# Kernel optimization log

Measured on AMD Instinct MI355X. Metric: run time of the kernel, lower is better.

The kernel has to match this reference:

```python
import jax, jax.numpy as jnp
import numpy as np

# static multi-scale feature pyramid (strides 8/16/32/64 of ~800px input)
SPATIAL = ((100, 100), (50, 50), (25, 25), (13, 13))
L = 4          # num_levels
NH = 8         # num_heads
NP = 4         # num_points
E = 256        # embed_dim
HD = E // NH   # head dim = 32
NLAYERS = 6
FFN_DIM = 1024
T = sum(h * w for h, w in SPATIAL)  # 13294 total tokens
B = 2


def _layer_norm(x, g, b, eps=1e-5):
    m = jnp.mean(x, -1, keepdims=True)
    v = jnp.mean((x - m) ** 2, -1, keepdims=True)
    return (x - m) * jax.lax.rsqrt(v + eps) * g + b


def _get_reference_points(valid_ratios):
    # valid_ratios: [B, L, 2] (wx, hy)
    refs = []
    for lvl, (H_, W_) in enumerate(SPATIAL):
        ry, rx = jnp.meshgrid(
            jnp.linspace(0.5, H_ - 0.5, H_, dtype=jnp.float32),
            jnp.linspace(0.5, W_ - 0.5, W_, dtype=jnp.float32),
            indexing='ij')
        ry = ry.reshape(-1)[None] / (valid_ratios[:, None, lvl, 1] * H_)
        rx = rx.reshape(-1)[None] / (valid_ratios[:, None, lvl, 0] * W_)
        refs.append(jnp.stack([rx, ry], -1))            # [B, H*W, 2]
    ref = jnp.concatenate(refs, 1)                       # [B, T, 2]
    return ref[:, :, None] * valid_ratios[:, None]       # [B, T, L, 2]


def _msda(value, loc, attn_w):
    # value: [B, T, NH, HD]; loc: [B, Q, NH, L, NP, 2] in [0,1]; attn_w: [B, Q, NH, L, NP]
    Bv, Tv, H, D = value.shape
    Q = loc.shape[1]
    out = jnp.zeros((Bv, Q, H, D), value.dtype)
    start = 0
    for lvl, (h, w) in enumerate(SPATIAL):
        v = value[:, start:start + h * w].transpose(0, 2, 1, 3)  # [B, NH, hw, D]
        start += h * w
        g = loc[:, :, :, lvl]                                    # [B, Q, NH, NP, 2]
        # grid_sample semantics, align_corners=False: pixel = g*size - 0.5
        x = g[..., 0] * w - 0.5
        y = g[..., 1] * h - 0.5
        x0 = jnp.floor(x).astype(jnp.int32)
        y0 = jnp.floor(y).astype(jnp.int32)
        wx = x - x0
        wy = y - y0

        def corner(ix, iy, cw):
            valid = (ix >= 0) & (ix < w) & (iy >= 0) & (iy < h)
            idx = jnp.clip(iy, 0, h - 1) * w + jnp.clip(ix, 0, w - 1)  # [B,Q,NH,NP]
            idx_t = idx.transpose(0, 2, 1, 3).reshape(Bv, H, Q * NP)
            gath = jnp.take_along_axis(v, idx_t[..., None], axis=2)    # [B,NH,QP,D]
            gath = gath.reshape(Bv, H, Q, NP, D)
            m = valid.transpose(0, 2, 1, 3)[..., None].astype(value.dtype)
            cw_t = cw.transpose(0, 2, 1, 3)[..., None]
            return gath * m * cw_t

        samp = (corner(x0, y0, (1 - wx) * (1 - wy))
                + corner(x0 + 1, y0, wx * (1 - wy))
                + corner(x0, y0 + 1, (1 - wx) * wy)
                + corner(x0 + 1, y0 + 1, wx * wy))  # [B,NH,Q,NP,D]
        out = out + jnp.einsum('bhqpd,bqhp->bqhd', samp, attn_w[:, :, :, lvl])
    return out.reshape(Bv, Q, H * D)


# offset normalizer (W, H) per level, as in Deformable-DETR
_OFF_NORM = jnp.array([[w, h] for (h, w) in SPATIAL], jnp.float32)  # [L, 2]


def _block(src, pos, ref, mask, p):
    (Wv, bv, Woff, boff, Wattn, battn, Wout, bout,
     n1g, n1b, n2g, n2b, W1, b1, W2, b2) = p
    x = _layer_norm(src, n1g, n1b)
    q = x + pos
    value = x @ Wv + bv
    value = jnp.where(mask[:, :, None], 0.0, value).reshape(B, T, NH, HD)
    off = (q @ Woff + boff).reshape(B, T, NH, L, NP, 2)
    attn = (q @ Wattn + battn).reshape(B, T, NH, L * NP)
    attn = jax.nn.softmax(attn, -1).reshape(B, T, NH, L, NP)
    loc = ref[:, :, None, :, None, :] + off / _OFF_NORM[None, None, None, :, None, :]
    attn_out = _msda(value, loc, attn) @ Wout + bout
    src = src + attn_out
    x = _layer_norm(src, n2g, n2b)
    ffn = jax.nn.relu(x @ W1 + b1) @ W2 + b2
    return src + ffn


def setup_inputs() -> dict:
    key = jax.random.key(0)
    ks = jax.random.split(key, 24)

    def rn(k, shape, scale=0.02):
        return jax.random.normal(k, shape, jnp.float32) * scale

    inp = {
        'src': jax.random.normal(ks[0], (B, T, E), jnp.float32),
        'pos': jax.random.normal(ks[1], (B, T, E), jnp.float32),
        'valid_ratios': jnp.ones((B, L, 2), jnp.float32),
        'spatial_shapes': jnp.array(SPATIAL, jnp.int32),
        'level_start_index': jnp.array(
            np.concatenate([[0], np.cumsum([h * w for h, w in SPATIAL])[:-1]]), jnp.int32),
        'mask': jnp.zeros((B, T), bool),
        # per-layer stacked parameters [NLAYERS, ...]
        'Wv': rn(ks[2], (NLAYERS, E, E)),
        'bv': jnp.zeros((NLAYERS, E), jnp.float32),
        'Woff': rn(ks[3], (NLAYERS, E, NH * L * NP * 2)),
        'boff': rn(ks[4], (NLAYERS, NH * L * NP * 2), 0.5),
        'Wattn': rn(ks[5], (NLAYERS, E, NH * L * NP)),
        'battn': jnp.zeros((NLAYERS, NH * L * NP), jnp.float32),
        'Wout': rn(ks[6], (NLAYERS, E, E)),
        'bout': jnp.zeros((NLAYERS, E), jnp.float32),
        'n1g': jnp.ones((NLAYERS, E), jnp.float32),
        'n1b': jnp.zeros((NLAYERS, E), jnp.float32),
        'n2g': jnp.ones((NLAYERS, E), jnp.float32),
        'n2b': jnp.zeros((NLAYERS, E), jnp.float32),
        'W1': rn(ks[7], (NLAYERS, E, FFN_DIM)),
        'b1': jnp.zeros((NLAYERS, FFN_DIM), jnp.float32),
        'W2': rn(ks[8], (NLAYERS, FFN_DIM, E)),
        'b2': jnp.zeros((NLAYERS, E), jnp.float32),
    }
    return inp


def reference(src, pos, valid_ratios, spatial_shapes, level_start_index, mask,
              Wv, bv, Woff, boff, Wattn, battn, Wout, bout,
              n1g, n1b, n2g, n2b, W1, b1, W2, b2):
    # spatial_shapes / level_start_index are encoded statically in SPATIAL (values match)
    ref = _get_reference_points(valid_ratios)  # [B, T, L, 2]
    x = src
    stacked = (Wv, bv, Woff, boff, Wattn, battn, Wout, bout,
               n1g, n1b, n2g, n2b, W1, b1, W2, b2)
    for i in range(NLAYERS):
        p = tuple(a[i] for a in stacked)
        x = _block(x, pos, ref, mask, p)
    return x
```

## Files before the change

### kernel.cpp

```cpp
#include <hip/hip_runtime.h>
#include <hip/hip_bf16.h>

#define NLAYERS 6
#define Bc 2
#define Tc 13294
#define Ec 256
#define NHc 8
#define FFNc 1024

#define EPI_BIAS 0
#define EPI_MASK 1
#define EPI_RES  2
#define EPI_RELU 3
#define EPI_VALOA 4

typedef __attribute__((ext_vector_type(8))) short bf16x8;
typedef __attribute__((ext_vector_type(4))) float f32x4;

typedef __attribute__((address_space(3))) unsigned int u32_lds;
typedef __attribute__((address_space(1))) unsigned int u32_glb;

__device__ __forceinline__ void gld16(const void* g, void* l) {
    __builtin_amdgcn_global_load_lds((const u32_glb*)g, (u32_lds*)l, 16, 0, 0);
}

__device__ __forceinline__ short f2bf(float f) {
    union { float f; unsigned u; } v; v.f = f;
    unsigned r = v.u + 0x7FFFu + ((v.u >> 16) & 1u);
    return (short)(r >> 16);
}
__device__ __forceinline__ float bf2f(short s) {
    union { unsigned u; float f; } v; v.u = ((unsigned)(unsigned short)s) << 16;
    return v.f;
}
__device__ __forceinline__ float bf_lo(unsigned u) {
    union { unsigned u; float f; } v; v.u = u << 16; return v.f;
}

__global__ __launch_bounds__(256) void f2bf_kernel(
    const float* __restrict__ in, short* __restrict__ out, int n4)
{
    int i = blockIdx.x * 256 + threadIdx.x;
    if (i >= n4) return;
    float4 v = *(const float4*)(in + (size_t)i * 4);
    short4 s; s.x = f2bf(v.x); s.y = f2bf(v.y); s.z = f2bf(v.z); s.w = f2bf(v.w);
    *(short4*)(out + (size_t)i * 4) = s;
}

__global__ __launch_bounds__(256) void ln_kernel(
    const float* __restrict__ src, const float* __restrict__ pos,
    const float* __restrict__ g, const float* __restrict__ b,
    short* __restrict__ x, short* __restrict__ q, int rows)
{
    int wave = threadIdx.x >> 6;
    int lane = threadIdx.x & 63;
    int row = blockIdx.x * 4 + wave;
    if (row >= rows) return;
    const float* p = src + (size_t)row * Ec;
    float4 v = *(const float4*)(p + lane * 4);
    float s  = v.x + v.y + v.z + v.w;
    float sq = v.x*v.x + v.y*v.y + v.z*v.z + v.w*v.w;
    #pragma unroll
    for (int o = 32; o; o >>= 1) { s += __shfl_xor(s, o); sq += __shfl_xor(sq, o); }
    float mean = s * (1.f / Ec);
    float var  = sq * (1.f / Ec) - mean * mean;
    float inv  = rsqrtf(var + 1e-5f);
    float4 gg = *(const float4*)(g + lane * 4);
    float4 bb = *(const float4*)(b + lane * 4);
    float xo0 = (v.x - mean) * inv * gg.x + bb.x;
    float xo1 = (v.y - mean) * inv * gg.y + bb.y;
    float xo2 = (v.z - mean) * inv * gg.z + bb.z;
    float xo3 = (v.w - mean) * inv * gg.w + bb.w;
    short4 xs; xs.x = f2bf(xo0); xs.y = f2bf(xo1); xs.z = f2bf(xo2); xs.w = f2bf(xo3);
    *(short4*)(x + (size_t)row * Ec + lane * 4) = xs;
    float4 pp = *(const float4*)(pos + (size_t)row * Ec + lane * 4);
    short4 qs;
    qs.x = f2bf(xo0 + pp.x); qs.y = f2bf(xo1 + pp.y);
    qs.z = f2bf(xo2 + pp.z); qs.w = f2bf(xo3 + pp.w);
    *(short4*)(q + (size_t)row * Ec + lane * 4) = qs;
}

__global__ __launch_bounds__(256) void ln_bf_kernel(
    const short* __restrict__ src, const short* __restrict__ pos,
    const float* __restrict__ g, const float* __restrict__ b,
    short* __restrict__ x, short* __restrict__ q, int rows)
{
    int wave = threadIdx.x >> 6;
    int lane = threadIdx.x & 63;
    int row = blockIdx.x * 4 + wave;
    if (row >= rows) return;
    short4 v4 = *(const short4*)(src + (size_t)row * Ec + lane * 4);
    float v0 = bf2f(v4.x), v1 = bf2f(v4.y), v2 = bf2f(v4.z), v3 = bf2f(v4.w);
    float s  = v0 + v1 + v2 + v3;
    float sq = v0*v0 + v1*v1 + v2*v2 + v3*v3;
    #pragma unroll
    for (int o = 32; o; o >>= 1) { s += __shfl_xor(s, o); sq += __shfl_xor(sq, o); }
    float mean = s * (1.f / Ec);
    float var  = sq * (1.f / Ec) - mean * mean;
    float inv  = rsqrtf(var + 1e-5f);
    float4 gg = *(const float4*)(g + lane * 4);
    float4 bb = *(const float4*)(b + lane * 4);
    float xo0 = (v0 - mean) * inv * gg.x + bb.x;
    float xo1 = (v1 - mean) * inv * gg.y + bb.y;
    float xo2 = (v2 - mean) * inv * gg.z + bb.z;
    float xo3 = (v3 - mean) * inv * gg.w + bb.w;
    short4 xs; xs.x = f2bf(xo0); xs.y = f2bf(xo1); xs.z = f2bf(xo2); xs.w = f2bf(xo3);
    *(short4*)(x + (size_t)row * Ec + lane * 4) = xs;
    if (q) {
        short4 pp = *(const short4*)(pos + (size_t)row * Ec + lane * 4);
        short4 qs;
        qs.x = f2bf(xo0 + bf2f(pp.x)); qs.y = f2bf(xo1 + bf2f(pp.y));
        qs.z = f2bf(xo2 + bf2f(pp.z)); qs.w = f2bf(xo3 + bf2f(pp.w));
        *(short4*)(q + (size_t)row * Ec + lane * 4) = qs;
    }
}

__global__ __launch_bounds__(256) void transpose_w(
    const float* __restrict__ W, short* __restrict__ Wt, int K, int N,
    int layerStride, int rowOff)
{
    __shared__ float tile[32][33];
    int l = blockIdx.z;
    const float* Wl = W + (size_t)l * K * N;
    short* Wtl = Wt + (size_t)l * layerStride;
    int n0 = blockIdx.x * 32, k0 = blockIdx.y * 32;
    int tx = threadIdx.x & 31, ty = threadIdx.x >> 5;
    #pragma unroll
    for (int i = 0; i < 32; i += 8)
        tile[ty + i][tx] = Wl[(size_t)(k0 + ty + i) * N + n0 + tx];
    __syncthreads();
    #pragma unroll
    for (int i = 0; i < 32; i += 8)
        Wtl[(size_t)(rowOff + n0 + ty + i) * K + k0 + tx] = f2bf(tile[tx][ty + i]);
}

template<int EPI, int OBF, int RESBF>
__global__ __launch_bounds__(256) void gemm_mfma(
    const short* __restrict__ A, const short* __restrict__ A2,
    const short* __restrict__ Bt,
    const float* __restrict__ bias, const float* __restrict__ bias2,
    const float* __restrict__ bias3,
    const float* __restrict__ resf, const short* __restrict__ resb,
    const unsigned char* __restrict__ mask,
    void* __restrict__ Cout, void* __restrict__ Cout2, int M, int N, int K)
{
    __shared__ short As[2][128 * 32];
    __shared__ short Bs[2][64 * 32];
    const int tid = threadIdx.x;
    const int lane = tid & 63;
    const int wv = tid >> 6;
    const int row0 = blockIdx.x * 128;
    const int col0 = blockIdx.y * 64;
    const int mbase = (wv >> 1) * 64;
    const int nbase = (wv & 1) * 32;
    const int lr = lane & 15;
    const int kg = lane >> 4;

    const short* Ause = (EPI == EPI_VALOA && blockIdx.y >= 4) ? A2 : A;

    f32x4 zf = {0.f, 0.f, 0.f, 0.f};
    f32x4 acc[4][2];
    #pragma unroll
    for (int i = 0; i < 4; ++i)
        #pragma unroll
        for (int j = 0; j < 2; ++j) acc[i][j] = zf;

    const int scol = (lane & 3) * 8;
    const int srowA = wv * 32 + (lane >> 2);
    const short* Ap = Ause + (size_t)(row0 + srowA) * K + scol;
    const int lA0 = srowA * 32 + scol;
    const int lA1 = lA0 + 16 * 32;
    const int srowB = wv * 16 + (lane >> 2);
    const short* Bp = Bt + (size_t)(col0 + srowB) * K + scol;
    const int lB = srowB * 32 + scol;

    #define STAGE(buf, k0) do { \
        gld16(Ap + (k0),                &As[buf][lA0]); \
        gld16(Ap + (size_t)16*K + (k0), &As[buf][lA1]); \
        gld16(Bp + (k0),                &Bs[buf][lB]); \
    } while (0)

    STAGE(0, 0);
    __syncthreads();
    int cur = 0;
    for (int k0 = 0; k0 < K; k0 += 32) {
        if (k0 + 32 < K) STAGE(cur ^ 1, k0 + 32);
        bf16x8 af[4], bfr[2];
        #pragma unroll
        for (int i = 0; i < 4; ++i)
            af[i]  = *(const bf16x8*)&As[cur][(mbase + i * 16 + lr) * 32 + kg * 8];
        #pragma unroll
        for (int j = 0; j < 2; ++j)
            bfr[j] = *(const bf16x8*)&Bs[cur][(nbase + j * 16 + lr) * 32 + kg * 8];
        #pragma unroll
        for (int mi = 0; mi < 4; ++mi)
            #pragma unroll
            for (int ni = 0; ni < 2; ++ni)
                acc[mi][ni] = __builtin_amdgcn_mfma_f32_16x16x32_bf16(
                    af[mi], bfr[ni], acc[mi][ni], 0, 0, 0);
        __syncthreads();
        cur ^= 1;
    }
    #undef STAGE

    float* Cf = (float*)Cout;
    short* Cb = (short*)Cout;
    short* Vb = (short*)Cout2;
    #pragma unroll
    for (int ni = 0; ni < 2; ++ni) {
        int col = col0 + nbase + ni * 16 + lr;
        float bz;
        if (EPI == EPI_VALOA)
            bz = (col < 256) ? bias[col] : ((col < 512) ? bias2[col - 256] : bias3[col - 512]);
        else
            bz = (bias2 && col >= 256) ? bias2[col - 256] : bias[col];
        #pragma unroll
        for (int mi = 0; mi < 4; ++mi) {
            int rb = row0 + mbase + mi * 16 + kg * 4;
            #pragma unroll
            for (int j = 0; j < 4; ++j) {
                int grow = rb + j;
                if (grow >= M) continue;
                float v = acc[mi][ni][j] + bz;
                if (EPI == EPI_VALOA) {
                    if (col < 256) {
                        if (mask[grow]) v = 0.f;
                        Vb[(size_t)grow * 256 + col] = f2bf(v);
                    } else {
                        Cb[(size_t)grow * 384 + (col - 256)] = f2bf(v);
                    }
                    continue;
                }
                if (EPI == EPI_MASK) { if (mask[grow]) v = 0.f; }
                if (EPI == EPI_RES) {
                    v += RESBF ? bf2f(resb[(size_t)grow * N + col])
                               : resf[(size_t)grow * N + col];
                }
                if (EPI == EPI_RELU) v = v > 0.f ? v : 0.f;
                if (OBF) Cb[(size_t)grow * N + col] = f2bf(v);
                else     Cf[(size_t)grow * N + col] = v;
            }
        }
    }
}

__global__ __launch_bounds__(256) void msda_kernel(
    const short* __restrict__ value, const short* __restrict__ oa,
    const float* __restrict__ vr, short* __restrict__ out)
{
    __shared__ int pts[8 * 136];
    const int t = threadIdx.x;
    const int bq = blockIdx.x;
    const int b = (bq >= Tc) ? 1 : 0;
    const int qq = bq - b * Tc;

    if (t < 128) {
        const int g = t >> 4;
        const int p = t & 15;
        const int lvl = p >> 2;
        const int Wl[4] = {100, 50, 25, 13};
        const int St[4] = {0, 10000, 12500, 13125};
        float base_x, base_y;
        if (qq < 10000) {
            int qi = qq;
            base_x = (0.5f + (float)(qi % 100)) / (vr[(b*4+0)*2+0] * 100.f);
            base_y = (0.5f + (float)(qi / 100)) / (vr[(b*4+0)*2+1] * 100.f);
        } else if (qq < 12500) {
            int qi = qq - 10000;
            base_x = (0.5f + (float)(qi % 50)) / (vr[(b*4+1)*2+0] * 50.f);
            base_y = (0.5f + (float)(qi / 50)) / (vr[(b*4+1)*2+1] * 50.f);
        } else if (qq < 13125) {
            int qi = qq - 12500;
            base_x = (0.5f + (float)(qi % 25)) / (vr[(b*4+2)*2+0] * 25.f);
            base_y = (0.5f + (float)(qi / 25)) / (vr[(b*4+2)*2+1] * 25.f);
        } else {
            int qi = qq - 13125;
            base_x = (0.5f + (float)(qi % 13)) / (vr[(b*4+3)*2+0] * 13.f);
            base_y = (0.5f + (float)(qi / 13)) / (vr[(b*4+3)*2+1] * 13.f);
        }
        float logit = bf2f(oa[(size_t)bq * 384 + 256 + g * 16 + p]);
        float mx = logit;
        #pragma unroll
        for (int o = 8; o; o >>= 1) mx = fmaxf(mx, __shfl_xor(mx, o));
        float e = expf(logit - mx);
        float sum = e;
        #pragma unroll
        for (int o = 8; o; o >>= 1) sum += __shfl_xor(sum, o);
        float aw = e / sum;

        const int w = Wl[lvl], hh = Wl[lvl];
        const float refx = base_x * vr[(b*4+lvl)*2+0];
        const float refy = base_y * vr[(b*4+lvl)*2+1];
        const float ox = bf2f(oa[(size_t)bq * 384 + g * 32 + p * 2 + 0]);
        const float oy = bf2f(oa[(size_t)bq * 384 + g * 32 + p * 2 + 1]);
        float locx = refx + ox / (float)w;
        float locy = refy + oy / (float)hh;
        float xf = locx * (float)w - 0.5f;
        float yf = locy * (float)hh - 0.5f;
        float x0f = floorf(xf), y0f = floorf(yf);
        int x0 = (int)x0f, y0 = (int)y0f;
        float wx = xf - x0f, wy = yf - y0f;
        float w00 = (1.f - wx) * (1.f - wy) * aw;
        float w10 = wx * (1.f - wy) * aw;
        float w01 = (1.f - wx) * wy * aw;
        float w11 = wx * wy * aw;
        bool vx0 = (x0 >= 0) && (x0 < w);
        bool vx1 = (x0 + 1 >= 0) && (x0 + 1 < w);
        bool vy0 = (y0 >= 0) && (y0 < hh);
        bool vy1 = (y0 + 1 >= 0) && (y0 + 1 < hh);
        if (!(vx0 && vy0)) w00 = 0.f;
        if (!(vx1 && vy0)) w10 = 0.f;
        if (!(vx0 && vy1)) w01 = 0.f;
        if (!(vx1 && vy1)) w11 = 0.f;
        int cx0 = min(max(x0, 0), w - 1), cx1 = min(max(x0 + 1, 0), w - 1);
        int cy0 = min(max(y0, 0), hh - 1), cy1 = min(max(y0 + 1, 0), hh - 1);
        int rowbase = b * Tc + St[lvl];
        int slot = g * 136 + p * 8 + ((p >> 3) & 1) * 4;
        int4 wq4; wq4.x = __float_as_int(w00); wq4.y = __float_as_int(w10);
        wq4.z = __float_as_int(w01); wq4.w = __float_as_int(w11);
        int4 aq4;
        aq4.x = (rowbase + cy0 * w + cx0) * 512 + g * 64;
        aq4.y = (rowbase + cy0 * w + cx1) * 512 + g * 64;
        aq4.z = (rowbase + cy1 * w + cx0) * 512 + g * 64;
        aq4.w = (rowbase + cy1 * w + cx1) * 512 + g * 64;
        *(int4*)&pts[slot] = wq4;
        *(int4*)&pts[slot + 4] = aq4;
    }
    __syncthreads();

    const int group = t >> 5;
    const int l32 = t & 31;
    const int d4 = (l32 & 15) * 4;
    const int ph = (l32 >> 4) * 8;
    const int xw = (l32 >> 4) * 4;
    const char* vbase = (const char*)value;
    float accL = 0.f, accH = 0.f;
    #pragma unroll
    for (int j = 0; j < 8; ++j) {
        int p = ph + j;
        int slot = group * 136 + p * 8 + xw;
        int4 wq = *(const int4*)&pts[slot];
        int4 aq = *(const int4*)&pts[slot + 4];
        unsigned u0 = *(const unsigned*)(vbase + (unsigned)(aq.x + d4));
        unsigned u1 = *(const unsigned*)(vbase + (unsigned)(aq.y + d4));
        unsigned u2 = *(const unsigned*)(vbase + (unsigned)(aq.z + d4));
        unsigned u3 = *(const unsigned*)(vbase + (unsigned)(aq.w + d4));
        float w00 = __int_as_float(wq.x), w10 = __int_as_float(wq.y);
        float w01 = __int_as_float(wq.z), w11 = __int_as_float(wq.w);
        accL = fmaf(w00, bf_lo(u0), accL); accH = fmaf(w00, __int_as_float((int)u0), accH);
        accL = fmaf(w10, bf_lo(u1), accL); accH = fmaf(w10, __int_as_float((int)u1), accH);
        accL = fmaf(w01, bf_lo(u2), accL); accH = fmaf(w01, __int_as_float((int)u2), accH);
        accL = fmaf(w11, bf_lo(u3), accL); accH = fmaf(w11, __int_as_float((int)u3), accH);
    }
    accL += __shfl_xor(accL, 16);
    accH += __shfl_xor(accH, 16);
    if (l32 < 16) {
        unsigned pk = ((unsigned)(unsigned short)f2bf(accL)) |
                      (((unsigned)(unsigned short)f2bf(accH)) << 16);
        *(unsigned*)((char*)out + (size_t)bq * 512 + group * 64 + d4) = pk;
    }
}

extern "C" void kernel_launch(void* const* d_in, const int* in_sizes, int n_in,
                              void* d_out, int out_size, void* d_ws, size_t ws_size,
                              hipStream_t stream) {
    const float* src  = (const float*)d_in[0];
    const float* pos  = (const float*)d_in[1];
    const float* vr   = (const float*)d_in[2];
    const unsigned char* mask = (const unsigned char*)d_in[5];
    const float* Wv    = (const float*)d_in[6];
    const float* bv    = (const float*)d_in[7];
    const float* Woff  = (const float*)d_in[8];
    const float* boff  = (const float*)d_in[9];
    const float* Wattn = (const float*)d_in[10];
    const float* battn = (const float*)d_in[11];
    const float* Wout  = (const float*)d_in[12];
    const float* bout  = (const float*)d_in[13];
    const float* n1g   = (const float*)d_in[14];
    const float* n1b   = (const float*)d_in[15];
    const float* n2g   = (const float*)d_in[16];
    const float* n2b   = (const float*)d_in[17];
    const float* W1    = (const float*)d_in[18];
    const float* b1    = (const float*)d_in[19];
    const float* W2    = (const float*)d_in[20];
    const float* b2    = (const float*)d_in[21];
    float* out = (float*)d_out;

    const size_t R = (size_t)Bc * Tc;

    short* xb    = (short*)d_ws;
    short* qb    = xb + R * 256;
    short* valb  = qb + R * 256;
    short* msdab = valb + R * 256;
    short* oab   = msdab + R * 256;
    short* srcb  = oab + R * 384;
    short* posb  = srcb + R * 256;
    short* ln2b  = xb;
    short* hb    = qb;
    short* wcT   = posb + R * 256;
    short* woutT = wcT + 6 * 163840;
    short* w1T   = woutT + 6 * 65536;
    short* w2T   = w1T + 6 * 262144;

    transpose_w<<<dim3(8, 8, 6),  256, 0, stream>>>(Wv,    wcT,   256, 256,  163840, 0);
    transpose_w<<<dim3(8, 8, 6),  256, 0, stream>>>(Woff,  wcT,   256, 256,  163840, 256);
    transpose_w<<<dim3(4, 8, 6),  256, 0, stream>>>(Wattn, wcT,   256, 128,  163840, 512);
    transpose_w<<<dim3(8, 8, 6),  256, 0, stream>>>(Wout,  woutT, 256, 256,  65536, 0);
    transpose_w<<<dim3(32, 8, 6), 256, 0, stream>>>(W1,    w1T,   256, 1024, 262144, 0);
    transpose_w<<<dim3(8, 32, 6), 256, 0, stream>>>(W2,    w2T,   1024, 256, 262144, 0);
    f2bf_kernel<<<(int)((R * 64 + 255) / 256), 256, 0, stream>>>(pos, posb, (int)(R * 64));

    const int M = (int)R;
    const int lnBlocks = (int)((R + 3) / 4);
    const int MT = (int)((R + 127) / 128);

    ln_kernel<<<lnBlocks, 256, 0, stream>>>(src, pos, n1g, n1b, xb, qb, M);

    for (int l = 0; l < NLAYERS; ++l) {
        gemm_mfma<EPI_VALOA, 1, 0><<<dim3(MT, 10), 256, 0, stream>>>(
            xb, qb, wcT + (size_t)l * 163840, bv + l * Ec, boff + l * 256, battn + l * 128,
            nullptr, nullptr, mask, oab, valb, M, 640, 256);
        msda_kernel<<<(int)R, 256, 0, stream>>>(valb, oab, vr, msdab);
        if (l == 0)
            gemm_mfma<EPI_RES, 1, 0><<<dim3(MT, 4), 256, 0, stream>>>(
                msdab, nullptr, woutT + (size_t)l * 65536, bout + l * Ec, nullptr, nullptr,
                src, nullptr, nullptr, srcb, nullptr, M, 256, 256);
        else
            gemm_mfma<EPI_RES, 1, 1><<<dim3(MT, 4), 256, 0, stream>>>(
                msdab, nullptr, woutT + (size_t)l * 65536, bout + l * Ec, nullptr, nullptr,
                nullptr, srcb, nullptr, srcb, nullptr, M, 256, 256);
        ln_bf_kernel<<<lnBlocks, 256, 0, stream>>>(srcb, nullptr, n2g + l * Ec, n2b + l * Ec,
                                                   ln2b, nullptr, M);
        gemm_mfma<EPI_RELU, 1, 0><<<dim3(MT, 16), 256, 0, stream>>>(
            ln2b, nullptr, w1T + (size_t)l * 262144, b1 + l * FFNc, nullptr, nullptr,
            nullptr, nullptr, nullptr, hb, nullptr, M, 1024, 256);
        if (l < NLAYERS - 1) {
            gemm_mfma<EPI_RES, 1, 1><<<dim3(MT, 4), 256, 0, stream>>>(
                hb, nullptr, w2T + (size_t)l * 262144, b2 + l * Ec, nullptr, nullptr,
                nullptr, srcb, nullptr, srcb, nullptr, M, 256, 1024);
            ln_bf_kernel<<<lnBlocks, 256, 0, stream>>>(srcb, posb, n1g + (l + 1) * Ec,
                                                       n1b + (l + 1) * Ec, xb, qb, M);
        } else {
            gemm_mfma<EPI_RES, 0, 1><<<dim3(MT, 4), 256, 0, stream>>>(
                hb, nullptr, w2T + (size_t)l * 262144, b2 + l * Ec, nullptr, nullptr,
                nullptr, srcb, nullptr, out, nullptr, M, 256, 1024);
        }
    }
}
```

Baseline: 1.151 ms.

## Add 128x128-tile GEMM for wide projections and widen MSDA value loads

Adds a gemm128 kernel with 128x128 output tiles (4x4 MFMA fragments per wave), used for the fused value/offset/attention projection and the FFN up-projection. The larger tiles give more reuse per staged A/B tile and halve the grid's column blocks. The MSDA sampling loop now loads 8 bytes per corner per lane instead of 4 and covers each head with 8 lanes, adding an extra shuffle-reduction step. The narrow-N GEMMs keep the slimmer 128x64 kernel. The cost is more accumulator registers, which may reduce occupancy.

```diff
diff --git a/kernel.cpp b/kernel.cpp
--- a/kernel.cpp
+++ b/kernel.cpp
@@ -136,13 +136,10 @@
 
 template<int EPI, int OBF, int RESBF>
 __global__ __launch_bounds__(256) void gemm_mfma(
-    const short* __restrict__ A, const short* __restrict__ A2,
-    const short* __restrict__ Bt,
-    const float* __restrict__ bias, const float* __restrict__ bias2,
-    const float* __restrict__ bias3,
+    const short* __restrict__ A, const short* __restrict__ Bt,
+    const float* __restrict__ bias,
     const float* __restrict__ resf, const short* __restrict__ resb,
-    const unsigned char* __restrict__ mask,
-    void* __restrict__ Cout, void* __restrict__ Cout2, int M, int N, int K)
+    void* __restrict__ Cout, int M, int N, int K)
 {
     __shared__ short As[2][128 * 32];
     __shared__ short Bs[2][64 * 32];
@@ -156,8 +153,6 @@
     const int lr = lane & 15;
     const int kg = lane >> 4;
 
-    const short* Ause = (EPI == EPI_VALOA && blockIdx.y >= 4) ? A2 : A;
-
     f32x4 zf = {0.f, 0.f, 0.f, 0.f};
     f32x4 acc[4][2];
     #pragma unroll
@@ -167,7 +162,7 @@
 
     const int scol = (lane & 3) * 8;
     const int srowA = wv * 32 + (lane >> 2);
-    const short* Ap = Ause + (size_t)(row0 + srowA) * K + scol;
+    const short* Ap = A + (size_t)(row0 + srowA) * K + scol;
     const int lA0 = srowA * 32 + scol;
     const int lA1 = lA0 + 16 * 32;
     const int srowB = wv * 16 + (lane >> 2);
@@ -205,15 +200,102 @@
 
     float* Cf = (float*)Cout;
     short* Cb = (short*)Cout;
-    short* Vb = (short*)Cout2;
     #pragma unroll
     for (int ni = 0; ni < 2; ++ni) {
+        int col = col0 + nbase + ni * 16 + lr;
+        float bz = bias[col];
+        #pragma unroll
+        for (int mi = 0; mi < 4; ++mi) {
+            int rb = row0 + mbase + mi * 16 + kg * 4;
+            #pragma unroll
+            for (int j = 0; j < 4; ++j) {
+                int grow = rb + j;
+                if (grow >= M) continue;
+                float v = acc[mi][ni][j] + bz;
+                if (EPI == EPI_RES) {
+                    v += RESBF ? bf2f(resb[(size_t)grow * N + col])
+                               : resf[(size_t)grow * N + col];
+                }
+                if (OBF) Cb[(size_t)grow * N + col] = f2bf(v);
+                else     Cf[(size_t)grow * N + col] = v;
+            }
+        }
+    }
+}
+
+template<int EPI>
+__global__ __launch_bounds__(256) void gemm128(
+    const short* __restrict__ A, const short* __restrict__ A2,
+    const short* __restrict__ Bt,
+    const float* __restrict__ bias, const float* __restrict__ bias2,
+    const float* __restrict__ bias3, const unsigned char* __restrict__ mask,
+    short* __restrict__ Cout, short* __restrict__ Vout, int M, int N, int K)
+{
+    __shared__ short As[2][128 * 32];
+    __shared__ short Bs[2][128 * 32];
+    const int tid = threadIdx.x;
+    const int lane = tid & 63;
+    const int wv = tid >> 6;
+    const int row0 = blockIdx.x * 128;
+    const int col0 = blockIdx.y * 128;
+    const int mbase = (wv >> 1) * 64;
+    const int nbase = (wv & 1) * 64;
+    const int lr = lane & 15;
+    const int kg = lane >> 4;
+
+    const short* Ause = (EPI == EPI_VALOA && blockIdx.y >= 2) ? A2 : A;
+
+    f32x4 zf = {0.f, 0.f, 0.f, 0.f};
+    f32x4 acc[4][4];
+    #pragma unroll
+    for (int i = 0; i < 4; ++i)
+        #pragma unroll
+        for (int j = 0; j < 4; ++j) acc[i][j] = zf;
+
+    const int scol = (lane & 3) * 8;
+    const int sr = wv * 32 + (lane >> 2);
+    const short* Ap = Ause + (size_t)(row0 + sr) * K + scol;
+    const short* Bp = Bt + (size_t)(col0 + sr) * K + scol;
+    const int l0 = sr * 32 + scol;
+    const int l1 = l0 + 16 * 32;
+
+    #define STAGE(buf, k0) do { \
+        gld16(Ap + (k0),                &As[buf][l0]); \
+        gld16(Ap + (size_t)16*K + (k0), &As[buf][l1]); \
+        gld16(Bp + (k0),                &Bs[buf][l0]); \
+        gld16(Bp + (size_t)16*K + (k0), &Bs[buf][l1]); \
+    } while (0)
+
+    STAGE(0, 0);
+    __syncthreads();
+    int cur = 0;
+    for (int k0 = 0; k0 < K; k0 += 32) {
+        if (k0 + 32 < K) STAGE(cur ^ 1, k0 + 32);
+        bf16x8 af[4], bfr[4];
+        #pragma unroll
+        for (int i = 0; i < 4; ++i) {
+            af[i]  = *(const bf16x8*)&As[cur][(mbase + i * 16 + lr) * 32 + kg * 8];
+            bfr[i] = *(const bf16x8*)&Bs[cur][(nbase + i * 16 + lr) * 32 + kg * 8];
+        }
+        #pragma unroll
+        for (int mi = 0; mi < 4; ++mi)
+            #pragma unroll
+            for (int ni = 0; ni < 4; ++ni)
+                acc[mi][ni] = __builtin_amdgcn_mfma_f32_16x16x32_bf16(
+                    af[mi], bfr[ni], acc[mi][ni], 0, 0, 0);
+        __syncthreads();
+        cur ^= 1;
+    }
+    #undef STAGE
+
+    #pragma unroll
+    for (int ni = 0; ni < 4; ++ni) {
         int col = col0 + nbase + ni * 16 + lr;
         float bz;
         if (EPI == EPI_VALOA)
             bz = (col < 256) ? bias[col] : ((col < 512) ? bias2[col - 256] : bias3[col - 512]);
         else
-            bz = (bias2 && col >= 256) ? bias2[col - 256] : bias[col];
+            bz = bias[col];
         #pragma unroll
         for (int mi = 0; mi < 4; ++mi) {
             int rb = row0 + mbase + mi * 16 + kg * 4;
@@ -225,20 +307,14 @@
                 if (EPI == EPI_VALOA) {
                     if (col < 256) {
                         if (mask[grow]) v = 0.f;
-                        Vb[(size_t)grow * 256 + col] = f2bf(v);
+                        Vout[(size_t)grow * 256 + col] = f2bf(v);
                     } else {
-                        Cb[(size_t)grow * 384 + (col - 256)] = f2bf(v);
+                        Cout[(size_t)grow * 384 + (col - 256)] = f2bf(v);
                     }
-                    continue;
+                } else {
+                    if (EPI == EPI_RELU) v = v > 0.f ? v : 0.f;
+                    Cout[(size_t)grow * N + col] = f2bf(v);
                 }
-                if (EPI == EPI_MASK) { if (mask[grow]) v = 0.f; }
-                if (EPI == EPI_RES) {
-                    v += RESBF ? bf2f(resb[(size_t)grow * N + col])
-                               : resf[(size_t)grow * N + col];
-                }
-                if (EPI == EPI_RELU) v = v > 0.f ? v : 0.f;
-                if (OBF) Cb[(size_t)grow * N + col] = f2bf(v);
-                else     Cf[(size_t)grow * N + col] = v;
             }
         }
     }
@@ -330,34 +406,43 @@
 
     const int group = t >> 5;
     const int l32 = t & 31;
-    const int d4 = (l32 & 15) * 4;
+    const int d8 = (l32 & 7) * 8;
     const int ph = (l32 >> 4) * 8;
-    const int xw = (l32 >> 4) * 4;
+    const int sub = (l32 >> 3) & 1;
     const char* vbase = (const char*)value;
-    float accL = 0.f, accH = 0.f;
-    #pragma unroll
-    for (int j = 0; j < 8; ++j) {
-        int p = ph + j;
-        int slot = group * 136 + p * 8 + xw;
+    float aL0 = 0.f, aH0 = 0.f, aL1 = 0.f, aH1 = 0.f;
+    #pragma unroll
+    for (int j = 0; j < 4; ++j) {
+        int p = ph + j * 2 + sub;
+        int slot = group * 136 + p * 8 + ((p >> 3) & 1) * 4;
         int4 wq = *(const int4*)&pts[slot];
         int4 aq = *(const int4*)&pts[slot + 4];
-        unsigned u0 = *(const unsigned*)(vbase + (unsigned)(aq.x + d4));
-        unsigned u1 = *(const unsigned*)(vbase + (unsigned)(aq.y + d4));
-        unsigned u2 = *(const unsigned*)(vbase + (unsigned)(aq.z + d4));
-        unsigned u3 = *(const unsigned*)(vbase + (unsigned)(aq.w + d4));
+        uint2 u0 = *(const uint2*)(vbase + (unsigned)(aq.x + d8));
+        uint2 u1 = *(const uint2*)(vbase + (unsigned)(aq.y + d8));
+        uint2 u2 = *(const uint2*)(vbase + (unsigned)(aq.z + d8));
+        uint2 u3 = *(const uint2*)(vbase + (unsigned)(aq.w + d8));
         float w00 = __int_as_float(wq.x), w10 = __int_as_float(wq.y);
         float w01 = __int_as_float(wq.z), w11 = __int_as_float(wq.w);
-        accL = fmaf(w00, bf_lo(u0), accL); accH = fmaf(w00, __int_as_float((int)u0), accH);
-        accL = fmaf(w10, bf_lo(u1), accL); accH = fmaf(w10, __int_as_float((int)u1), accH);
-        accL = fmaf(w01, bf_lo(u2), accL); accH = fmaf(w01, __int_as_float((int)u2), accH);
-        accL = fmaf(w11, bf_lo(u3), accL); accH = fmaf(w11, __int_as_float((int)u3), accH);
-    }
-    accL += __shfl_xor(accL, 16);
-    accH += __shfl_xor(accH, 16);
-    if (l32 < 16) {
-        unsigned pk = ((unsigned)(unsigned short)f2bf(accL)) |
-                      (((unsigned)(unsigned short)f2bf(accH)) << 16);
-        *(unsigned*)((char*)out + (size_t)bq * 512 + group * 64 + d4) = pk;
+        aL0 = fmaf(w00, bf_lo(u0.x), aL0); aH0 = fmaf(w00, __int_as_float((int)u0.x), aH0);
+        aL1 = fmaf(w00, bf_lo(u0.y), aL1); aH1 = fmaf(w00, __int_as_float((int)u0.y), aH1);
+        aL0 = fmaf(w10, bf_lo(u1.x), aL0); aH0 = fmaf(w10, __int_as_float((int)u1.x), aH0);
+        aL1 = fmaf(w10, bf_lo(u1.y), aL1); aH1 = fmaf(w10, __int_as_float((int)u1.y), aH1);
+        aL0 = fmaf(w01, bf_lo(u2.x), aL0); aH0 = fmaf(w01, __int_as_float((int)u2.x), aH0);
+        aL1 = fmaf(w01, bf_lo(u2.y), aL1); aH1 = fmaf(w01, __int_as_float((int)u2.y), aH1);
+        aL0 = fmaf(w11, bf_lo(u3.x), aL0); aH0 = fmaf(w11, __int_as_float((int)u3.x), aH0);
+        aL1 = fmaf(w11, bf_lo(u3.y), aL1); aH1 = fmaf(w11, __int_as_float((int)u3.y), aH1);
+    }
+    aL0 += __shfl_xor(aL0, 8);  aH0 += __shfl_xor(aH0, 8);
+    aL1 += __shfl_xor(aL1, 8);  aH1 += __shfl_xor(aH1, 8);
+    aL0 += __shfl_xor(aL0, 16); aH0 += __shfl_xor(aH0, 16);
+    aL1 += __shfl_xor(aL1, 16); aH1 += __shfl_xor(aH1, 16);
+    if (l32 < 8) {
+        uint2 pk;
+        pk.x = ((unsigned)(unsigned short)f2bf(aL0)) |
+               (((unsigned)(unsigned short)f2bf(aH0)) << 16);
+        pk.y = ((unsigned)(unsigned short)f2bf(aL1)) |
+               (((unsigned)(unsigned short)f2bf(aH1)) << 16);
+        *(uint2*)((char*)out + (size_t)bq * 512 + group * 64 + d8) = pk;
     }
 }
 
@@ -417,33 +502,33 @@
     ln_kernel<<<lnBlocks, 256, 0, stream>>>(src, pos, n1g, n1b, xb, qb, M);
 
     for (int l = 0; l < NLAYERS; ++l) {
-        gemm_mfma<EPI_VALOA, 1, 0><<<dim3(MT, 10), 256, 0, stream>>>(
+        gemm128<EPI_VALOA><<<dim3(MT, 5), 256, 0, stream>>>(
             xb, qb, wcT + (size_t)l * 163840, bv + l * Ec, boff + l * 256, battn + l * 128,
-            nullptr, nullptr, mask, oab, valb, M, 640, 256);
+            mask, oab, valb, M, 640, 256);
         msda_kernel<<<(int)R, 256, 0, stream>>>(valb, oab, vr, msdab);
         if (l == 0)
             gemm_mfma<EPI_RES, 1, 0><<<dim3(MT, 4), 256, 0, stream>>>(
-                msdab, nullptr, woutT + (size_t)l * 65536, bout + l * Ec, nullptr, nullptr,
-                src, nullptr, nullptr, srcb, nullptr, M, 256, 256);
+                msdab, woutT + (size_t)l * 65536, bout + l * Ec, src, nullptr,
+                srcb, M, 256, 256);
         else
             gemm_mfma<EPI_RES, 1, 1><<<dim3(MT, 4), 256, 0, stream>>>(
-                msdab, nullptr, woutT + (size_t)l * 65536, bout + l * Ec, nullptr, nullptr,
-                nullptr, srcb, nullptr, srcb, nullptr, M, 256, 256);
+                msdab, woutT + (size_t)l * 65536, bout + l * Ec, nullptr, srcb,
+                srcb, M, 256, 256);
         ln_bf_kernel<<<lnBlocks, 256, 0, stream>>>(srcb, nullptr, n2g + l * Ec, n2b + l * Ec,
                                                    ln2b, nullptr, M);
-        gemm_mfma<EPI_RELU, 1, 0><<<dim3(MT, 16), 256, 0, stream>>>(
+        gemm128<EPI_RELU><<<dim3(MT, 8), 256, 0, stream>>>(
             ln2b, nullptr, w1T + (size_t)l * 262144, b1 + l * FFNc, nullptr, nullptr,
-            nullptr, nullptr, nullptr, hb, nullptr, M, 1024, 256);
+            nullptr, hb, nullptr, M, 1024, 256);
         if (l < NLAYERS - 1) {
             gemm_mfma<EPI_RES, 1, 1><<<dim3(MT, 4), 256, 0, stream>>>(
-                hb, nullptr, w2T + (size_t)l * 262144, b2 + l * Ec, nullptr, nullptr,
-                nullptr, srcb, nullptr, srcb, nullptr, M, 256, 1024);
+                hb, w2T + (size_t)l * 262144, b2 + l * Ec, nullptr, srcb,
+                srcb, M, 256, 1024);
             ln_bf_kernel<<<lnBlocks, 256, 0, stream>>>(srcb, posb, n1g + (l + 1) * Ec,
                                                        n1b + (l + 1) * Ec, xb, qb, M);
         } else {
             gemm_mfma<EPI_RES, 0, 1><<<dim3(MT, 4), 256, 0, stream>>>(
-                hb, nullptr, w2T + (size_t)l * 262144, b2 + l * Ec, nullptr, nullptr,
-                nullptr, srcb, nullptr, out, nullptr, M, 256, 1024);
+                hb, w2T + (size_t)l * 262144, b2 + l * Ec, nullptr, srcb,
+                out, M, 256, 1024);
         }
     }
 }
```

After: 1.331 ms. +15.6%, slower.
